# Optimization experiments

Measured on AMD Instinct MI355X. Metric: run time of the kernel, lower is better.

The kernel has to match this reference:

```python
import jax, jax.numpy as jnp
import numpy as np

K = 3  # PyG TAGConv default number of hops


def _gcn_norm(edge_index, num_nodes):
    # Symmetric GCN normalization WITHOUT self-loops (TAGConv default).
    row, col = edge_index[0], edge_index[1]
    w = jnp.ones(edge_index.shape[1], dtype=jnp.float32)
    deg = jax.ops.segment_sum(w, col, num_segments=num_nodes)
    dinv = jnp.where(deg > 0, jax.lax.rsqrt(jnp.maximum(deg, 1.0)), 0.0)
    return dinv[row] * dinv[col]  # [E]


def _tagconv(x, edge_index, norm, W, b):
    # W: [K+1, d_in, d_out], b: [d_out]
    row, col = edge_index[0], edge_index[1]
    n = x.shape[0]
    out = x @ W[0]
    h = x
    for k in range(1, K + 1):
        # h <- D^-1/2 A D^-1/2 h  via gather + segment-sum scatter
        h = jax.ops.segment_sum(norm[:, None] * h[row], col, num_segments=n)
        out = out + h @ W[k]
    return out + b


def setup_inputs() -> dict:
    key = jax.random.key(0)
    k1, k2, k3, k4, k5, k6 = jax.random.split(key, 6)
    N, E = 100000, 1600000
    d_in, d_hid, d_out = 64, 64, 40
    x = jax.random.normal(k1, (N, d_in), dtype=jnp.float32)
    edge_index = jax.random.randint(k2, (2, E), 0, N, dtype=jnp.int32)
    s1 = 1.0 / np.sqrt(d_in)
    s2 = 1.0 / np.sqrt(d_hid)
    W1 = jax.random.uniform(k3, (K + 1, d_in, d_hid), jnp.float32, -s1, s1)
    b1 = jnp.zeros((d_hid,), jnp.float32)
    W2 = jax.random.uniform(k4, (K + 1, d_hid, d_out), jnp.float32, -s2, s2)
    b2 = jnp.zeros((d_out,), jnp.float32)
    return {"x": x, "edge_index": edge_index, "W1": W1, "b1": b1, "W2": W2, "b2": b2}


def reference(x, edge_index, W1, b1, W2, b2):
    norm = _gcn_norm(edge_index, x.shape[0])
    h = jax.nn.relu(_tagconv(x, edge_index, norm, W1, b1))
    # F.dropout in eval mode: identity
    h = _tagconv(h, edge_index, norm, W2, b2)
    return jax.nn.log_softmax(h, axis=1)
```

## Files before the change

kernel.cpp:

```cpp
#include <hip/hip_runtime.h>
#include <math.h>

#define DIN 64
#define NB_MAX 512
#define S1_CHUNK 4096

typedef unsigned short us8 __attribute__((ext_vector_type(8)));
typedef short s16x8 __attribute__((ext_vector_type(8)));
typedef float f32x4 __attribute__((ext_vector_type(4)));


__device__ __forceinline__ float bf2f(unsigned short u) {
    return __uint_as_float(((unsigned int)u) << 16);
}
__device__ __forceinline__ unsigned short f2bf(float f) {
    unsigned int u = __float_as_uint(f);
    return (unsigned short)((u + 0x7fffu + ((u >> 16) & 1u)) >> 16);
}


__global__ __launch_bounds__(256) void bcount_kernel(const int* __restrict__ col,
                                                     int* __restrict__ bcnt, int E, int NB) {
    __shared__ int cntB[NB_MAX];
    for (int t = threadIdx.x; t < NB; t += 256) cntB[t] = 0;
    __syncthreads();
    int stride = gridDim.x * blockDim.x;
    for (int i = blockIdx.x * blockDim.x + threadIdx.x; i < E; i += stride)
        atomicAdd(&cntB[col[i] >> 8], 1);
    __syncthreads();
    for (int t = threadIdx.x; t < NB; t += 256) {
        int c = cntB[t];
        if (c) atomicAdd(&bcnt[t], c);
    }
}

__global__ void bscan_kernel(const int* __restrict__ bcnt, int* __restrict__ bbase,
                             int* __restrict__ gcur, int* __restrict__ rowptr,
                             int NB, int N, int E) {
    __shared__ int sm[512];
    int tid = threadIdx.x;
    int v = (tid < NB) ? bcnt[tid] : 0;
    sm[tid] = v;
    __syncthreads();
    for (int off = 1; off < 512; off <<= 1) {
        int add = (tid >= off) ? sm[tid - off] : 0;
        __syncthreads();
        sm[tid] += add;
        __syncthreads();
    }
    if (tid < NB) { int b = sm[tid] - v; bbase[tid] = b; gcur[tid] = b; }
    if (tid == NB - 1) bbase[NB] = sm[tid];
    if (tid == 0) rowptr[N] = E;
}


__global__ __launch_bounds__(256) void s1_bucket(const int* __restrict__ row,
                                                 const int* __restrict__ col,
                                                 int* __restrict__ gcur,
                                                 int* __restrict__ sorted, int E, int NB) {
    __shared__ int2 ebuf[S1_CHUNK];
    __shared__ int cntL[NB_MAX];
    __shared__ int baseL[NB_MAX];
    __shared__ int curL[NB_MAX];
    __shared__ int gbaseL[NB_MAX];
    __shared__ int sm[256];
    int tid = threadIdx.x;
    int jb = blockIdx.x * S1_CHUNK;
    int je = min(jb + S1_CHUNK, E);
    int cntTot = je - jb;

    for (int t = tid; t < NB; t += 256) cntL[t] = 0;
    __syncthreads();
    for (int j = jb + tid; j < je; j += 256) atomicAdd(&cntL[col[j] >> 8], 1);
    __syncthreads();
    int per = (NB + 255) >> 8;
    int s = 0;
    for (int q = 0; q < per; ++q) {
        int idx = tid * per + q;
        if (idx < NB) s += cntL[idx];
    }
    sm[tid] = s;
    __syncthreads();
    for (int off = 1; off < 256; off <<= 1) {
        int add = (tid >= off) ? sm[tid - off] : 0;
        __syncthreads();
        sm[tid] += add;
        __syncthreads();
    }
    int run = sm[tid] - s;
    for (int q = 0; q < per; ++q) {
        int idx = tid * per + q;
        if (idx < NB) { baseL[idx] = run; curL[idx] = run; run += cntL[idx]; }
    }
    __syncthreads();
    for (int t = tid; t < NB; t += 256)
        gbaseL[t] = atomicAdd(&gcur[t], cntL[t]);
    for (int j = jb + tid; j < je; j += 256) {
        int c = col[j];
        int pos = atomicAdd(&curL[c >> 8], 1);
        ebuf[pos] = make_int2(row[j], c);
    }
    __syncthreads();
    for (int jj = tid; jj < cntTot; jj += 256) {
        int2 e = ebuf[jj];
        int t = e.y >> 8;
        sorted[gbaseL[t] + (jj - baseL[t])] = (e.x << 8) | (e.y & 255);
    }
}


__global__ __launch_bounds__(256) void s2_kernel(const int* __restrict__ sorted,
                                                 const int* __restrict__ bbase,
                                                 int* __restrict__ rowptr,
                                                 float* __restrict__ dinv,
                                                 float* __restrict__ rdinv,
                                                 int* __restrict__ srcarr, int N) {
    __shared__ int cntL[256], baseL[256], sm[256];
    int tid = threadIdx.x;
    int b = blockIdx.x;
    int c0 = b << 8;
    int nLoc = min(256, N - c0);
    int gs = bbase[b], ge = bbase[b + 1];
    cntL[tid] = 0;
    __syncthreads();
    for (int j = gs + tid; j < ge; j += 256)
        atomicAdd(&cntL[sorted[j] & 255], 1);
    __syncthreads();
    int c = cntL[tid];
    sm[tid] = c;
    __syncthreads();
    for (int off = 1; off < 256; off <<= 1) {
        int add = (tid >= off) ? sm[tid - off] : 0;
        __syncthreads();
        sm[tid] += add;
        __syncthreads();
    }
    int base = gs + sm[tid] - c;
    baseL[tid] = base;
    if (tid < nLoc) {
        rowptr[c0 + tid] = base;
        dinv[c0 + tid] = (c > 0) ? rsqrtf((float)c) : 0.0f;
        rdinv[c0 + tid] = (c > 0) ? sqrtf((float)c) : 0.0f;
    }
    cntL[tid] = 0;
    __syncthreads();
    for (int j = gs + tid; j < ge; j += 256) {
        int e = sorted[j];
        int cl = e & 255;
        int p = baseL[cl] + atomicAdd(&cntL[cl], 1);
        srcarr[p] = e >> 8;
    }
}


__global__ void cvt_kernel(const float* __restrict__ x, const float* __restrict__ dinv,
                           unsigned short* __restrict__ hb0, unsigned short* __restrict__ sb0,
                           int n4) {
    int i = blockIdx.x * blockDim.x + threadIdx.x;
    if (i >= n4) return;
    float d = dinv[i >> 4];
    float4 v = *(const float4*)&x[(size_t)i * 4];
    ushort4 h, s;
    h.x = f2bf(v.x); h.y = f2bf(v.y); h.z = f2bf(v.z); h.w = f2bf(v.w);
    s.x = f2bf(d * v.x); s.y = f2bf(d * v.y); s.z = f2bf(d * v.z); s.w = f2bf(d * v.w);
    *(ushort4*)&hb0[(size_t)i * 4] = h;
    *(ushort4*)&sb0[(size_t)i * 4] = s;
}


__global__ __launch_bounds__(256) void prop_kernel(const int* __restrict__ rowptr,
                                                   const int* __restrict__ srcarr,
                                                   const float* __restrict__ dinv,
                                                   const unsigned short* __restrict__ sb_in,
                                                   unsigned short* __restrict__ sb_out, int N) {
    int gid = blockIdx.x * blockDim.x + threadIdx.x;
    int node = gid >> 6;
    if (node >= N) return;
    int lane = threadIdx.x & 63;
    int g = lane >> 3, l = lane & 7;
    int beg = rowptr[node], end = rowptr[node + 1];
    int deg = end - beg;
    float a[8] = {};
    for (int chunk = 0; chunk < deg; chunk += 64) {
        int lim = min(64, deg - chunk);
        int src_l = (lane < lim) ? srcarr[beg + chunk + lane] : 0;
        int iters = (lim + 7) >> 3;
        for (int t = 0; t < iters; ++t) {
            int jj = g + (t << 3);
            int src = __shfl(src_l, jj, 64);
            if (jj < lim) {
                us8 hv = *(const us8*)&sb_in[(size_t)src * DIN + l * 8];
#pragma unroll
                for (int k = 0; k < 8; ++k) a[k] += bf2f(hv[k]);
            }
        }
    }
#pragma unroll
    for (int off = 8; off < 64; off <<= 1) {
#pragma unroll
        for (int k = 0; k < 8; ++k) a[k] += __shfl_xor(a[k], off, 64);
    }
    if (g == 0) {
        float d = dinv[node];
        float d2 = d * d;
        us8 o;
#pragma unroll
        for (int k = 0; k < 8; ++k) o[k] = f2bf(d2 * a[k]);
        *(us8*)&sb_out[(size_t)node * DIN + l * 8] = o;
    }
}


template <bool ADDIN>
__global__ __launch_bounds__(256) void prop40_kernel(const int* __restrict__ rowptr,
                                                     const int* __restrict__ srcarr,
                                                     const float* __restrict__ dinv,
                                                     const unsigned short* __restrict__ in,
                                                     const unsigned short* __restrict__ addin,
                                                     unsigned short* __restrict__ out, int N) {
    int gid = blockIdx.x * blockDim.x + threadIdx.x;
    int node = gid >> 6;
    if (node >= N) return;
    int lane = threadIdx.x & 63;
    int g = lane >> 3, l = lane & 7;
    int beg = rowptr[node], end = rowptr[node + 1];
    int deg = end - beg;
    float a[8] = {};
    for (int chunk = 0; chunk < deg; chunk += 64) {
        int lim = min(64, deg - chunk);
        int src_l = (lane < lim) ? srcarr[beg + chunk + lane] : 0;
        int iters = (lim + 7) >> 3;
        for (int t = 0; t < iters; ++t) {
            int jj = g + (t << 3);
            int src = __shfl(src_l, jj, 64);
            if (jj < lim && l < 5) {
                us8 hv = *(const us8*)&in[(size_t)src * 40 + l * 8];
#pragma unroll
                for (int k = 0; k < 8; ++k) a[k] += bf2f(hv[k]);
            }
        }
    }
#pragma unroll
    for (int off = 8; off < 64; off <<= 1) {
#pragma unroll
        for (int k = 0; k < 8; ++k) a[k] += __shfl_xor(a[k], off, 64);
    }
    if (g == 0 && l < 5) {
        float d = dinv[node];
        float d2 = d * d;
        us8 o;
        if (ADDIN) {
            us8 ad = *(const us8*)&addin[(size_t)node * 40 + l * 8];
#pragma unroll
            for (int k = 0; k < 8; ++k) o[k] = f2bf(bf2f(ad[k]) + d2 * a[k]);
        } else {
#pragma unroll
            for (int k = 0; k < 8; ++k) o[k] = f2bf(d2 * a[k]);
        }
        *(us8*)&out[(size_t)node * 40 + l * 8] = o;
    }
}


__global__ void wprep_kernel(const float* __restrict__ W, unsigned short* __restrict__ Wb,
                             int DOUTsrc, int CT) {
    int idx = blockIdx.x * blockDim.x + threadIdx.x;
    int total = 4 * 2 * CT * 64;
    if (idx >= total) return;
    int lane = idx & 63;
    int rest = idx >> 6;
    int ct = rest % CT;
    int tmp = rest / CT;
    int ks = tmp & 1, kk = tmp >> 1;
    int colc = ct * 16 + (lane & 15);
    int k0 = ks * 32 + (lane >> 4) * 8;
    us8 ov;
#pragma unroll
    for (int j = 0; j < 8; ++j) {
        float v = (colc < DOUTsrc) ? W[(size_t)(kk * 64 + k0 + j) * DOUTsrc + colc] : 0.0f;
        ov[j] = f2bf(v);
    }
    *(us8*)&Wb[(size_t)idx * 8] = ov;
}


template <int CT, int MODE>
__global__ __launch_bounds__(256) void mm4m_kernel(const unsigned short* __restrict__ h0,
                                                   const unsigned short* __restrict__ s1,
                                                   const unsigned short* __restrict__ s2,
                                                   const unsigned short* __restrict__ s3,
                                                   const float* __restrict__ rdinv,
                                                   const float* __restrict__ dinv,
                                                   const unsigned short* __restrict__ Wb,
                                                   const float* __restrict__ bias,
                                                   float* __restrict__ outf,
                                                   unsigned short* __restrict__ outh,
                                                   unsigned short* __restrict__ outs, int N) {
    constexpr int LSTR = (MODE == 2) ? 68 : 52;
    __shared__ __align__(16) float Lds[64 * LSTR];
    int tid = threadIdx.x;
    int w = tid >> 6, lane = tid & 63;
    int row0 = blockIdx.x * 64 + w * 16;
    int arow = row0 + (lane & 15);
    bool aok = arow < N;
    size_t abase = (size_t)arow * DIN + ((lane >> 4) * 8);
    const unsigned short* hp[4] = {h0, s1, s2, s3};

    f32x4 acc0[CT] = {};
    f32x4 accS[CT] = {};
#pragma unroll
    for (int kk = 0; kk < 4; ++kk) {
        const unsigned short* hb = hp[kk];
#pragma unroll
        for (int ks = 0; ks < 2; ++ks) {
            s16x8 a = {};
            if (aok) a = *(const s16x8*)&hb[abase + ks * 32];
#pragma unroll
            for (int c = 0; c < CT; ++c) {
                s16x8 b = *(const s16x8*)&Wb[(size_t)(((kk * 2 + ks) * CT + c) * 64 + lane) * 8];
                if (kk == 0)
                    acc0[c] = __builtin_amdgcn_mfma_f32_16x16x32_bf16(a, b, acc0[c], 0, 0, 0);
                else
                    accS[c] = __builtin_amdgcn_mfma_f32_16x16x32_bf16(a, b, accS[c], 0, 0, 0);
            }
        }
    }
    int lcol = lane & 15;
    int lrow4 = (lane >> 4) * 4;
#pragma unroll
    for (int r = 0; r < 4; ++r) {
        int lr = lrow4 + r;
        int grow = row0 + lr;
        float rd = (grow < N) ? rdinv[grow] : 0.0f;
#pragma unroll
        for (int c = 0; c < CT; ++c) {
            float v = acc0[c][r] + rd * accS[c][r];
            if (MODE == 2) {
                v += bias[c * 16 + lcol];
                v = v > 0.0f ? v : 0.0f;
            }
            Lds[(w * 16 + lr) * LSTR + c * 16 + lcol] = v;
        }
    }
    __syncthreads();
    int rowsInBlk = min(64, N - blockIdx.x * 64);
    if (MODE == 2) {
        for (int idx = tid; idx < rowsInBlk * 8; idx += 256) {
            int r = idx >> 3, k8 = (idx & 7) * 8;
            int gr = blockIdx.x * 64 + r;
            us8 oh;
#pragma unroll
            for (int k = 0; k < 8; ++k) oh[k] = f2bf(Lds[r * LSTR + k8 + k]);
            *(us8*)&outh[(size_t)gr * DIN + k8] = oh;
            if (outs != nullptr) {
                float d = dinv[gr];
                us8 os;
#pragma unroll
                for (int k = 0; k < 8; ++k) os[k] = f2bf(d * Lds[r * LSTR + k8 + k]);
                *(us8*)&outs[(size_t)gr * DIN + k8] = os;
            }
        }
    } else {
        for (int idx = tid; idx < rowsInBlk * 10; idx += 256) {
            int r = idx / 10, c4 = idx - r * 10;
            int gr = blockIdx.x * 64 + r;
            float4 v = *(float4*)&Lds[r * LSTR + c4 * 4];
            *(float4*)&outf[(size_t)gr * 40 + c4 * 4] = v;
        }
    }
}


__global__ __launch_bounds__(256) void mmU_kernel(const unsigned short* __restrict__ P,
                                                  const float* __restrict__ dinv,
                                                  const unsigned short* __restrict__ Wb,
                                                  float* __restrict__ u0f,
                                                  unsigned short* __restrict__ u1,
                                                  unsigned short* __restrict__ u2,
                                                  unsigned short* __restrict__ u3, int N) {
    constexpr int CT = 3, LSTR = 52;
    __shared__ __align__(16) float Lds[64 * LSTR];
    int tid = threadIdx.x;
    int w = tid >> 6, lane = tid & 63;
    int row0 = blockIdx.x * 64 + w * 16;
    int arow = row0 + (lane & 15);
    bool aok = arow < N;
    size_t abase = (size_t)arow * DIN + ((lane >> 4) * 8);
    s16x8 a0 = {}, a1 = {};
    if (aok) {
        a0 = *(const s16x8*)&P[abase];
        a1 = *(const s16x8*)&P[abase + 32];
    }
    f32x4 acc[4][CT] = {};
#pragma unroll
    for (int kk = 0; kk < 4; ++kk) {
#pragma unroll
        for (int c = 0; c < CT; ++c) {
            s16x8 b0 = *(const s16x8*)&Wb[(size_t)(((kk * 2 + 0) * CT + c) * 64 + lane) * 8];
            s16x8 b1 = *(const s16x8*)&Wb[(size_t)(((kk * 2 + 1) * CT + c) * 64 + lane) * 8];
            acc[kk][c] = __builtin_amdgcn_mfma_f32_16x16x32_bf16(a0, b0, acc[kk][c], 0, 0, 0);
            acc[kk][c] = __builtin_amdgcn_mfma_f32_16x16x32_bf16(a1, b1, acc[kk][c], 0, 0, 0);
        }
    }
    int lcol = lane & 15;
    int lrow4 = (lane >> 4) * 4;
    int rowsInBlk = min(64, N - blockIdx.x * 64);
    unsigned short* up[4] = {nullptr, u1, u2, u3};
#pragma unroll
    for (int kk = 0; kk < 4; ++kk) {
#pragma unroll
        for (int r = 0; r < 4; ++r)
#pragma unroll
            for (int c = 0; c < CT; ++c)
                Lds[(w * 16 + lrow4 + r) * LSTR + c * 16 + lcol] = acc[kk][c][r];
        __syncthreads();
        if (kk == 0) {
            for (int idx = tid; idx < rowsInBlk * 10; idx += 256) {
                int r = idx / 10, c4 = idx - r * 10;
                int gr = blockIdx.x * 64 + r;
                float4 v = *(float4*)&Lds[r * LSTR + c4 * 4];
                *(float4*)&u0f[(size_t)gr * 40 + c4 * 4] = v;
            }
        } else {
            unsigned short* u = up[kk];
            for (int idx = tid; idx < rowsInBlk * 5; idx += 256) {
                int r = idx / 5, seg = idx - r * 5;
                int gr = blockIdx.x * 64 + r;
                float d = dinv[gr];
                us8 o;
#pragma unroll
                for (int k = 0; k < 8; ++k) o[k] = f2bf(d * Lds[r * LSTR + seg * 8 + k]);
                *(us8*)&u[(size_t)gr * 40 + seg * 8] = o;
            }
        }
        __syncthreads();
    }
}


__global__ void lsm_kernel(float* __restrict__ out, const unsigned short* __restrict__ t,
                           const float* __restrict__ rdinv, const float* __restrict__ bias,
                           int N) {
    int gid = blockIdx.x * blockDim.x + threadIdx.x;
    int row = gid >> 6;
    int lane = gid & 63;
    if (row >= N) return;
    float rd = rdinv[row];
    float v = -INFINITY;
    if (lane < 40)
        v = out[(size_t)row * 40 + lane] + rd * bf2f(t[(size_t)row * 40 + lane]) + bias[lane];
    float m = v;
    for (int off = 32; off > 0; off >>= 1) m = fmaxf(m, __shfl_xor(m, off, 64));
    float e = (lane < 40) ? expf(v - m) : 0.0f;
    float ssum = e;
    for (int off = 32; off > 0; off >>= 1) ssum += __shfl_xor(ssum, off, 64);
    if (lane < 40) out[(size_t)row * 40 + lane] = v - m - logf(ssum);
}


extern "C" void kernel_launch(void* const* d_in, const int* in_sizes, int n_in,
                              void* d_out, int out_size, void* d_ws, size_t ws_size,
                              hipStream_t stream) {
    const float* x  = (const float*)d_in[0];
    const int*   ei = (const int*)d_in[1];
    const float* W1 = (const float*)d_in[2];
    const float* b1 = (const float*)d_in[3];
    const float* W2 = (const float*)d_in[4];
    const float* b2 = (const float*)d_in[5];

    int N = in_sizes[0] / DIN;
    int E = in_sizes[1] / 2;
    const int* rowv = ei;
    const int* colv = ei + E;
    int NB = (N + 255) >> 8;

    char* p = (char*)d_ws;
    auto alloc = [&](size_t bytes) {
        char* q = p;
        p += (bytes + 255) & ~(size_t)255;
        return q;
    };
    int*   bcnt   = (int*)alloc(NB_MAX * 4);
    int*   bbase  = (int*)alloc((NB_MAX + 1) * 4);
    int*   gcur   = (int*)alloc(NB_MAX * 4);
    int*   rowptr = (int*)alloc((size_t)(N + 1) * 4);
    float* dinv   = (float*)alloc((size_t)N * 4);
    float* rdinv  = (float*)alloc((size_t)N * 4);
    int*   sorted = (int*)alloc((size_t)E * 4);
    int*   srcarr = (int*)alloc((size_t)E * 4);
    unsigned short* Wb1 = (unsigned short*)alloc((size_t)4 * 2 * 4 * 64 * 8 * 2);
    unsigned short* Wb2 = (unsigned short*)alloc((size_t)4 * 2 * 3 * 64 * 8 * 2);
    unsigned short* hb0 = (unsigned short*)alloc((size_t)N * DIN * 2);
    unsigned short* hbE = (unsigned short*)alloc((size_t)N * DIN * 2);
    unsigned short* sbA = (unsigned short*)alloc((size_t)N * DIN * 2);
    unsigned short* sbB = (unsigned short*)alloc((size_t)N * DIN * 2);
    unsigned short* sbC = (unsigned short*)alloc((size_t)N * DIN * 2);
    unsigned short* sbD = (unsigned short*)alloc((size_t)N * DIN * 2);
    unsigned short* u1  = (unsigned short*)alloc((size_t)N * 40 * 2);
    unsigned short* u2  = (unsigned short*)alloc((size_t)N * 40 * 2);
    unsigned short* u3  = (unsigned short*)alloc((size_t)N * 40 * 2);
    unsigned short* t40A = (unsigned short*)alloc((size_t)N * 40 * 2);
    unsigned short* t40B = (unsigned short*)alloc((size_t)N * 40 * 2);
    float* outp   = (float*)d_out;

    hipMemsetAsync(bcnt, 0, NB_MAX * 4, stream);

    const int tpb = 256;

    bcount_kernel<<<128, tpb, 0, stream>>>(colv, bcnt, E, NB);
    bscan_kernel<<<1, 512, 0, stream>>>(bcnt, bbase, gcur, rowptr, NB, N, E);
    s1_bucket<<<(E + S1_CHUNK - 1) / S1_CHUNK, 256, 0, stream>>>(rowv, colv, gcur, sorted, E, NB);
    s2_kernel<<<NB, 256, 0, stream>>>(sorted, bbase, rowptr, dinv, rdinv, srcarr, N);
    wprep_kernel<<<8, tpb, 0, stream>>>(W1, Wb1, 64, 4);
    wprep_kernel<<<6, tpb, 0, stream>>>(W2, Wb2, 40, 3);

    int propBlocks = (N * 64 + tpb - 1) / tpb;
    int mmBlocks = (N + 63) / 64;
    int n4 = N * 16;
    cvt_kernel<<<(n4 + tpb - 1) / tpb, tpb, 0, stream>>>(x, dinv, hb0, sbA, n4);

    prop_kernel<<<propBlocks, tpb, 0, stream>>>(rowptr, srcarr, dinv, sbA, sbB, N);
    prop_kernel<<<propBlocks, tpb, 0, stream>>>(rowptr, srcarr, dinv, sbB, sbC, N);
    prop_kernel<<<propBlocks, tpb, 0, stream>>>(rowptr, srcarr, dinv, sbC, sbD, N);
    mm4m_kernel<4, 2><<<mmBlocks, 256, 0, stream>>>(hb0, sbB, sbC, sbD, rdinv, dinv,
                                                    Wb1, b1, nullptr, hbE, nullptr, N);

    mmU_kernel<<<mmBlocks, 256, 0, stream>>>(hbE, dinv, Wb2, outp, u1, u2, u3, N);
    prop40_kernel<true><<<propBlocks, tpb, 0, stream>>>(rowptr, srcarr, dinv, u3, u2, t40A, N);
    prop40_kernel<true><<<propBlocks, tpb, 0, stream>>>(rowptr, srcarr, dinv, t40A, u1, t40B, N);
    prop40_kernel<false><<<propBlocks, tpb, 0, stream>>>(rowptr, srcarr, dinv, t40B, nullptr, t40A, N);
    lsm_kernel<<<propBlocks, tpb, 0, stream>>>(outp, t40A, rdinv, b2, N);
}
```

Before: 394.5 us.

## Bucket edges by destination block and source slab to improve gather locality

The edge bucketing now keys on destination block times source slab (32K-row slabs). Within each destination bucket, edges are grouped by source range, so the later CSR propagation gathers should touch source rows with better cache locality. To fit the larger segment tables in shared memory, the bucket tables grow to 2048 entries, the S1 chunk size is halved and the scan kernels handle several segments per thread. This adds preprocessing work and more blocks, and the gain depends on whether s2's per-destination placement keeps the slab order.

```diff
diff --git a/kernel.cpp b/kernel.cpp
--- a/kernel.cpp
+++ b/kernel.cpp
@@ -2,8 +2,9 @@
 #include <math.h>
 
 #define DIN 64
-#define NB_MAX 512
-#define S1_CHUNK 4096
+#define SEG_MAX 2048
+#define S1_CHUNK 2048
+#define SLAB_SHIFT 15
 
 typedef unsigned short us8 __attribute__((ext_vector_type(8)));
 typedef short s16x8 __attribute__((ext_vector_type(8)));
@@ -19,16 +20,21 @@
 }
 
 
-__global__ __launch_bounds__(256) void bcount_kernel(const int* __restrict__ col,
-                                                     int* __restrict__ bcnt, int E, int NB) {
-    __shared__ int cntB[NB_MAX];
-    for (int t = threadIdx.x; t < NB; t += 256) cntB[t] = 0;
+__global__ __launch_bounds__(256) void bcount_kernel(const int* __restrict__ row,
+                                                     const int* __restrict__ col,
+                                                     int* __restrict__ bcnt,
+                                                     int E, int NS) {
+    __shared__ int cntB[SEG_MAX];
+    int NSEG_loc = SEG_MAX;
+    for (int t = threadIdx.x; t < NSEG_loc; t += 256) cntB[t] = 0;
     __syncthreads();
     int stride = gridDim.x * blockDim.x;
-    for (int i = blockIdx.x * blockDim.x + threadIdx.x; i < E; i += stride)
-        atomicAdd(&cntB[col[i] >> 8], 1);
-    __syncthreads();
-    for (int t = threadIdx.x; t < NB; t += 256) {
+    for (int i = blockIdx.x * blockDim.x + threadIdx.x; i < E; i += stride) {
+        int seg = (col[i] >> 8) * NS + (row[i] >> SLAB_SHIFT);
+        atomicAdd(&cntB[seg], 1);
+    }
+    __syncthreads();
+    for (int t = threadIdx.x; t < NSEG_loc; t += 256) {
         int c = cntB[t];
         if (c) atomicAdd(&bcnt[t], c);
     }
@@ -36,11 +42,16 @@
 
 __global__ void bscan_kernel(const int* __restrict__ bcnt, int* __restrict__ bbase,
                              int* __restrict__ gcur, int* __restrict__ rowptr,
-                             int NB, int N, int E) {
+                             int NSEG, int N, int E) {
     __shared__ int sm[512];
     int tid = threadIdx.x;
-    int v = (tid < NB) ? bcnt[tid] : 0;
-    sm[tid] = v;
+    int per = (NSEG + 511) >> 9;
+    int s = 0;
+    for (int q = 0; q < per; ++q) {
+        int idx = tid * per + q;
+        if (idx < NSEG) s += bcnt[idx];
+    }
+    sm[tid] = s;
     __syncthreads();
     for (int off = 1; off < 512; off <<= 1) {
         int add = (tid >= off) ? sm[tid - off] : 0;
@@ -48,8 +59,12 @@
         sm[tid] += add;
         __syncthreads();
     }
-    if (tid < NB) { int b = sm[tid] - v; bbase[tid] = b; gcur[tid] = b; }
-    if (tid == NB - 1) bbase[NB] = sm[tid];
+    int run = sm[tid] - s;
+    for (int q = 0; q < per; ++q) {
+        int idx = tid * per + q;
+        if (idx < NSEG) { bbase[idx] = run; gcur[idx] = run; run += bcnt[idx]; }
+    }
+    if (tid == 511) bbase[NSEG] = sm[511];
     if (tid == 0) rowptr[N] = E;
 }
 
@@ -57,27 +72,31 @@
 __global__ __launch_bounds__(256) void s1_bucket(const int* __restrict__ row,
                                                  const int* __restrict__ col,
                                                  int* __restrict__ gcur,
-                                                 int* __restrict__ sorted, int E, int NB) {
+                                                 int* __restrict__ sorted,
+                                                 int E, int NS, int NSEG) {
     __shared__ int2 ebuf[S1_CHUNK];
-    __shared__ int cntL[NB_MAX];
-    __shared__ int baseL[NB_MAX];
-    __shared__ int curL[NB_MAX];
-    __shared__ int gbaseL[NB_MAX];
+    __shared__ int cntL[SEG_MAX];
+    __shared__ int baseL[SEG_MAX];
+    __shared__ int curL[SEG_MAX];
+    __shared__ int gbaseL[SEG_MAX];
     __shared__ int sm[256];
     int tid = threadIdx.x;
     int jb = blockIdx.x * S1_CHUNK;
     int je = min(jb + S1_CHUNK, E);
     int cntTot = je - jb;
 
-    for (int t = tid; t < NB; t += 256) cntL[t] = 0;
-    __syncthreads();
-    for (int j = jb + tid; j < je; j += 256) atomicAdd(&cntL[col[j] >> 8], 1);
-    __syncthreads();
-    int per = (NB + 255) >> 8;
+    for (int t = tid; t < NSEG; t += 256) cntL[t] = 0;
+    __syncthreads();
+    for (int j = jb + tid; j < je; j += 256) {
+        int seg = (col[j] >> 8) * NS + (row[j] >> SLAB_SHIFT);
+        atomicAdd(&cntL[seg], 1);
+    }
+    __syncthreads();
+    int per = (NSEG + 255) >> 8;
     int s = 0;
     for (int q = 0; q < per; ++q) {
         int idx = tid * per + q;
-        if (idx < NB) s += cntL[idx];
+        if (idx < NSEG) s += cntL[idx];
     }
     sm[tid] = s;
     __syncthreads();
@@ -90,21 +109,21 @@
     int run = sm[tid] - s;
     for (int q = 0; q < per; ++q) {
         int idx = tid * per + q;
-        if (idx < NB) { baseL[idx] = run; curL[idx] = run; run += cntL[idx]; }
-    }
-    __syncthreads();
-    for (int t = tid; t < NB; t += 256)
+        if (idx < NSEG) { baseL[idx] = run; curL[idx] = run; run += cntL[idx]; }
+    }
+    __syncthreads();
+    for (int t = tid; t < NSEG; t += 256)
         gbaseL[t] = atomicAdd(&gcur[t], cntL[t]);
     for (int j = jb + tid; j < je; j += 256) {
-        int c = col[j];
-        int pos = atomicAdd(&curL[c >> 8], 1);
-        ebuf[pos] = make_int2(row[j], c);
+        int r = row[j], c = col[j];
+        int seg = (c >> 8) * NS + (r >> SLAB_SHIFT);
+        int pos = atomicAdd(&curL[seg], 1);
+        ebuf[pos] = make_int2((r << 8) | (c & 255), seg);
     }
     __syncthreads();
     for (int jj = tid; jj < cntTot; jj += 256) {
         int2 e = ebuf[jj];
-        int t = e.y >> 8;
-        sorted[gbaseL[t] + (jj - baseL[t])] = (e.x << 8) | (e.y & 255);
+        sorted[gbaseL[e.y] + (jj - baseL[e.y])] = e.x;
     }
 }
 
@@ -114,13 +133,13 @@
                                                  int* __restrict__ rowptr,
                                                  float* __restrict__ dinv,
                                                  float* __restrict__ rdinv,
-                                                 int* __restrict__ srcarr, int N) {
+                                                 int* __restrict__ srcarr, int N, int NS) {
     __shared__ int cntL[256], baseL[256], sm[256];
     int tid = threadIdx.x;
     int b = blockIdx.x;
     int c0 = b << 8;
     int nLoc = min(256, N - c0);
-    int gs = bbase[b], ge = bbase[b + 1];
+    int gs = bbase[b * NS], ge = bbase[b * NS + NS];
     cntL[tid] = 0;
     __syncthreads();
     for (int j = gs + tid; j < ge; j += 256)
@@ -473,6 +492,8 @@
     const int* rowv = ei;
     const int* colv = ei + E;
     int NB = (N + 255) >> 8;
+    int NS = ((N - 1) >> SLAB_SHIFT) + 1;
+    int NSEG = NB * NS;
 
     char* p = (char*)d_ws;
     auto alloc = [&](size_t bytes) {
@@ -480,9 +501,9 @@
         p += (bytes + 255) & ~(size_t)255;
         return q;
     };
-    int*   bcnt   = (int*)alloc(NB_MAX * 4);
-    int*   bbase  = (int*)alloc((NB_MAX + 1) * 4);
-    int*   gcur   = (int*)alloc(NB_MAX * 4);
+    int*   bcnt   = (int*)alloc(SEG_MAX * 4);
+    int*   bbase  = (int*)alloc((SEG_MAX + 1) * 4);
+    int*   gcur   = (int*)alloc(SEG_MAX * 4);
     int*   rowptr = (int*)alloc((size_t)(N + 1) * 4);
     float* dinv   = (float*)alloc((size_t)N * 4);
     float* rdinv  = (float*)alloc((size_t)N * 4);
@@ -503,14 +524,14 @@
     unsigned short* t40B = (unsigned short*)alloc((size_t)N * 40 * 2);
     float* outp   = (float*)d_out;
 
-    hipMemsetAsync(bcnt, 0, NB_MAX * 4, stream);
+    hipMemsetAsync(bcnt, 0, SEG_MAX * 4, stream);
 
     const int tpb = 256;
 
-    bcount_kernel<<<128, tpb, 0, stream>>>(colv, bcnt, E, NB);
-    bscan_kernel<<<1, 512, 0, stream>>>(bcnt, bbase, gcur, rowptr, NB, N, E);
-    s1_bucket<<<(E + S1_CHUNK - 1) / S1_CHUNK, 256, 0, stream>>>(rowv, colv, gcur, sorted, E, NB);
-    s2_kernel<<<NB, 256, 0, stream>>>(sorted, bbase, rowptr, dinv, rdinv, srcarr, N);
+    bcount_kernel<<<128, tpb, 0, stream>>>(rowv, colv, bcnt, E, NS);
+    bscan_kernel<<<1, 512, 0, stream>>>(bcnt, bbase, gcur, rowptr, NSEG, N, E);
+    s1_bucket<<<(E + S1_CHUNK - 1) / S1_CHUNK, 256, 0, stream>>>(rowv, colv, gcur, sorted, E, NS, NSEG);
+    s2_kernel<<<NB, 256, 0, stream>>>(sorted, bbase, rowptr, dinv, rdinv, srcarr, N, NS);
     wprep_kernel<<<8, tpb, 0, stream>>>(W1, Wb1, 64, 4);
     wprep_kernel<<<6, tpb, 0, stream>>>(W2, Wb2, 40, 3);
 
```

New measurement: 420.2 us. +6.5%, slower.
